# Optimization experiments

Measured on AMD Instinct MI355X. Metric: run time of the kernel, lower is better.

Reference implementation:

```python
import jax, jax.numpy as jnp
import numpy as np

WS = 8      # window_size
SS = 4      # shift_size
DIM = 192
HEADS = 6
N = WS * WS
EPS = 1e-5


def _rel_pos_index():
    coords = np.stack(np.meshgrid(np.arange(WS), np.arange(WS), indexing='ij')).reshape(2, -1)
    rel = (coords[:, :, None] - coords[:, None, :]).transpose(1, 2, 0)  # [N,N,2]
    rel[..., 0] += WS - 1
    rel[..., 1] += WS - 1
    rel[..., 0] *= 2 * WS - 1
    return rel.sum(-1)  # [N,N] int


def _attn_mask(H, W):
    img = np.zeros((H, W))
    sl = (slice(0, -WS), slice(-WS, -SS), slice(-SS, None))
    cnt = 0
    for hs in sl:
        for ws_ in sl:
            img[hs, ws_] = cnt
            cnt += 1
    mw = img.reshape(H // WS, WS, W // WS, WS).transpose(0, 2, 1, 3).reshape(-1, N)
    d = mw[:, None, :] - mw[:, :, None]
    return np.where(d != 0, -100.0, 0.0).astype(np.float32)  # [nW,N,N]


def _ln(x, g, b):
    m = x.mean(-1, keepdims=True)
    v = ((x - m) ** 2).mean(-1, keepdims=True)
    return (x - m) / jnp.sqrt(v + EPS) * g + b


def setup_inputs() -> dict:
    key = jax.random.key(0)
    ks = jax.random.split(key, 12)
    C, Hd = DIM, DIM * 4
    s = 0.02
    return {
        'x': jax.random.normal(ks[0], (2, 256, 256, C), dtype=jnp.float32),
        'norm1_g': jnp.ones((C,), jnp.float32),
        'norm1_b': jnp.zeros((C,), jnp.float32),
        'qkv_w': jax.random.normal(ks[1], (3 * C, C), jnp.float32) * s,
        'rpb_table': jax.random.normal(ks[2], ((2 * WS - 1) ** 2, HEADS), jnp.float32) * s,
        'proj_w': jax.random.normal(ks[3], (C, C), jnp.float32) * s,
        'proj_b': jnp.zeros((C,), jnp.float32),
        'norm2_g': jnp.ones((C,), jnp.float32),
        'norm2_b': jnp.zeros((C,), jnp.float32),
        'mlp_w1': jax.random.normal(ks[4], (Hd, C), jnp.float32) * s,
        'mlp_b1': jnp.zeros((Hd,), jnp.float32),
        'mlp_w2': jax.random.normal(ks[5], (C, Hd), jnp.float32) * s,
        'mlp_b2': jnp.zeros((C,), jnp.float32),
    }


def reference(x, norm1_g, norm1_b, qkv_w, rpb_table, proj_w, proj_b,
              norm2_g, norm2_b, mlp_w1, mlp_b1, mlp_w2, mlp_b2):
    B, H, W, C = x.shape
    hd = C // HEADS
    shortcut = x
    xn = _ln(x, norm1_g, norm1_b)
    xs = jnp.roll(xn, (-SS, -SS), axis=(1, 2))
    # window partition -> [B_*nW, N, C]
    xw = xs.reshape(B, H // WS, WS, W // WS, WS, C).transpose(0, 1, 3, 2, 4, 5).reshape(-1, N, C)
    B_ = xw.shape[0]
    qkv = (xw @ qkv_w.T).reshape(B_, N, 3, HEADS, hd).transpose(2, 0, 3, 1, 4)
    q, k, v = qkv[0] * (hd ** -0.5), qkv[1], qkv[2]
    attn = jnp.einsum('bhid,bhjd->bhij', q, k)  # [B_,H,N,N]
    rpi = jnp.asarray(_rel_pos_index().reshape(-1))
    bias = rpb_table[rpi].reshape(N, N, HEADS).transpose(2, 0, 1)  # [H,N,N]
    attn = attn + bias[None]
    mask = jnp.asarray(_attn_mask(H, W))  # [nW,N,N]
    nW = mask.shape[0]
    attn = (attn.reshape(B_ // nW, nW, HEADS, N, N) + mask[None, :, None]).reshape(B_, HEADS, N, N)
    attn = jax.nn.softmax(attn, axis=-1)
    out = jnp.einsum('bhij,bhjd->bhid', attn, v).transpose(0, 2, 1, 3).reshape(B_, N, C)
    out = out @ proj_w.T + proj_b
    # window reverse + roll back
    out = out.reshape(B, H // WS, W // WS, WS, WS, C).transpose(0, 1, 3, 2, 4, 5).reshape(B, H, W, C)
    x1 = shortcut + jnp.roll(out, (SS, SS), axis=(1, 2))
    h = _ln(x1, norm2_g, norm2_b)
    h = jax.nn.gelu(h @ mlp_w1.T + mlp_b1, approximate=False)
    h = h @ mlp_w2.T + mlp_b2
    return x1 + h
```

## Files before the change

kernel.cpp:

```cpp
#include <hip/hip_runtime.h>
#include <hip/hip_bf16.h>
#include <math.h>

typedef unsigned short u16;
typedef unsigned int u32;
typedef __attribute__((ext_vector_type(8))) short short8;
typedef __attribute__((ext_vector_type(4))) float floatx4;

__device__ __forceinline__ float bf2f(u16 u) { return __uint_as_float(((u32)u) << 16); }
__device__ __forceinline__ u16 f2bf(float f) {
  u32 u = __float_as_uint(f);
  u32 r = u + 0x7fffu + ((u >> 16) & 1u);
  return (u16)(r >> 16);
}

#define WSB_OFF  0
#define WSQ_OFF  393216
#define WSP_OFF  614400
#define WSM1_OFF 688128
#define WSM2_OFF 983040

__global__ __launch_bounds__(256) void k_prep(
    const float* __restrict__ qkvw, const float* __restrict__ projw,
    const float* __restrict__ rpb,
    const float* __restrict__ w1, const float* __restrict__ w2,
    float* __restrict__ wsb, u16* __restrict__ wsq, u16* __restrict__ wsp,
    u16* __restrict__ wsm1, u16* __restrict__ wsm2)
{
  const int tid0 = blockIdx.x * 256 + threadIdx.x;
  const int NT = gridDim.x * 256;
  for (int idx = tid0; idx < 110592; idx += NT) {
    int e = idx & 7, lane = (idx >> 3) & 63, rest = idx >> 9;
    int s = rest % 6, T = rest / 6;
    int mat = T / 12, hct = T % 12;
    int row = mat * 192 + hct * 16 + (lane & 15);
    int col = 32 * s + 8 * (lane >> 4) + e;
    float v = qkvw[(size_t)row * 192 + col];
    if (mat == 0) v *= 0.1767766952966369f;
    wsq[idx] = f2bf(v);
  }
  for (int idx = tid0; idx < 36864; idx += NT) {
    int e = idx & 7, lane = (idx >> 3) & 63, rest = idx >> 9;
    int nt = rest % 12, h = rest / 12;
    int row = 16 * nt + (lane & 15);
    int col = 32 * h + 8 * (lane >> 4) + e;
    wsp[idx] = f2bf(projw[(size_t)row * 192 + col]);
  }
  for (int idx = tid0; idx < 147456; idx += NT) {
    int e = idx & 7, lane = (idx >> 3) & 63, rest = idx >> 9;
    int s = rest % 6, t = rest / 6;
    int n = t & 1, ch = t >> 1;
    wsm1[idx] = f2bf(w1[(size_t)(ch * 32 + n * 16 + (lane & 15)) * 192
                        + 32 * s + 8 * (lane >> 4) + e]);
  }
  for (int idx = tid0; idx < 147456; idx += NT) {
    int e = idx & 7, lane = (idx >> 3) & 63, rest = idx >> 9;
    int ct = rest % 12, ch = rest / 12;
    wsm2[idx] = f2bf(w2[(size_t)(ct * 16 + (lane & 15)) * 768
                        + ch * 32 + 8 * (lane >> 4) + e]);
  }
  for (int idx = tid0; idx < 98304; idx += NT) {
    int f16 = idx & 15; int nt = f16 >> 2, r = f16 & 3;
    int t = (idx >> 4) & 255; int rest = idx >> 12;
    int h = rest % 6, cat = rest / 6;
    int w = t >> 6, m = t & 15, ql = (t >> 4) & 3;
    int i = 16 * w + 4 * ql + r, j = 16 * nt + m;
    int ir = i >> 3, ic = i & 7, jr = j >> 3, jc = j & 7;
    float v = rpb[((ir - jr + 7) * 15 + (ic - jc + 7)) * 6 + h];
    int catH = cat >> 1, catW = cat & 1;
    int ci = (catH ? ((ir < 4) ? 1 : 2) : 0) * 3 + (catW ? ((ic < 4) ? 1 : 2) : 0);
    int cj = (catH ? ((jr < 4) ? 1 : 2) : 0) * 3 + (catW ? ((jc < 4) ? 1 : 2) : 0);
    if (ci != cj) v -= 100.f;
    wsb[idx] = v;
  }
}

__global__ __launch_bounds__(256, 3) void k_fused(
    const float* __restrict__ x,
    const float* __restrict__ g1, const float* __restrict__ b1,
    const float* __restrict__ projb,
    const float* __restrict__ wsb, const u16* __restrict__ wsq,
    const u16* __restrict__ wsp,
    const float* __restrict__ g2, const float* __restrict__ b2,
    const u16* __restrict__ wsm1, const float* __restrict__ bm1,
    const u16* __restrict__ wsm2, const float* __restrict__ bm2,
    float* __restrict__ out)
{
  __shared__ __align__(16) u16 xnA[12800];
  __shared__ __align__(16) u16 pool[12288];
  const int QS = 0, KS = 2560, VT = 5120, POB = 7424;

  const int tid = threadIdx.x;
  const int blk = blockIdx.x;
  const int b  = blk >> 10;
  const int wh = (blk >> 5) & 31;
  const int ww = blk & 31;

  {
    const int t = tid >> 2, l4 = tid & 3;
    const int rr = t >> 3, cc = t & 7;
    const int oh = (wh * 8 + rr + 4) & 255;
    const int ow = (ww * 8 + cc + 4) & 255;
    const float* px = x + (((size_t)b * 65536 + (size_t)oh * 256 + ow) * 192) + l4 * 48;
    float rv[48];
    float s = 0.f, ss = 0.f;
    const float4* p4 = (const float4*)px;
    #pragma unroll
    for (int i = 0; i < 12; ++i) {
      float4 v = p4[i];
      rv[i*4+0] = v.x; rv[i*4+1] = v.y; rv[i*4+2] = v.z; rv[i*4+3] = v.w;
      s  += v.x + v.y + v.z + v.w;
      ss += v.x*v.x + v.y*v.y + v.z*v.z + v.w*v.w;
    }
    s += __shfl_xor(s, 1);  s += __shfl_xor(s, 2);
    ss += __shfl_xor(ss, 1); ss += __shfl_xor(ss, 2);
    const float mean = s * (1.f / 192.f);
    const float var  = ss * (1.f / 192.f) - mean * mean;
    const float rstd = rsqrtf(var + 1e-5f);
    const int c0 = l4 * 48;
    #pragma unroll
    for (int i = 0; i < 12; ++i) {
      ushort4 o;
      o.x = f2bf((rv[i*4+0] - mean) * rstd * g1[c0+i*4+0] + b1[c0+i*4+0]);
      o.y = f2bf((rv[i*4+1] - mean) * rstd * g1[c0+i*4+1] + b1[c0+i*4+1]);
      o.z = f2bf((rv[i*4+2] - mean) * rstd * g1[c0+i*4+2] + b1[c0+i*4+2]);
      o.w = f2bf((rv[i*4+3] - mean) * rstd * g1[c0+i*4+3] + b1[c0+i*4+3]);
      *(ushort4*)&xnA[t * 200 + c0 + i*4] = o;
    }
  }

  const int w    = tid >> 6;
  const int lane = tid & 63;
  const int m    = tid & 15;
  const int ql   = (tid >> 4) & 3;
  const int ct   = w >> 1;
  const int tb   = (w & 1) * 2;
  const int cat  = ((wh == 31) ? 2 : 0) | ((ww == 31) ? 1 : 0);
  const float* pbias = wsb + ((size_t)(cat * 6) * 256 + tid) * 16;
  const int po = POB + w * 1152;

  floatx4 acc[12];
  #pragma unroll
  for (int nt = 0; nt < 12; ++nt) acc[nt] = (floatx4){0.f, 0.f, 0.f, 0.f};

  __syncthreads();

  #pragma unroll 1
  for (int h = 0; h < 6; ++h) {
    {
      const u16* wqp = wsq + (size_t)(h * 2 + ct) * 3072 + lane * 8;
      floatx4 dq[2], dk[2], dv[2];
      #pragma unroll
      for (int t = 0; t < 2; ++t) {
        dq[t] = (floatx4){0.f,0.f,0.f,0.f};
        dk[t] = (floatx4){0.f,0.f,0.f,0.f};
        dv[t] = (floatx4){0.f,0.f,0.f,0.f};
      }
      #pragma unroll
      for (int s = 0; s < 6; ++s) {
        short8 a0 = *(const short8*)&xnA[(16*tb + m) * 200 + 32*s + 8*ql];
        short8 a1 = *(const short8*)&xnA[(16*tb + 16 + m) * 200 + 32*s + 8*ql];
        short8 bq = *(const short8*)(wqp + s*512);
        short8 bk = *(const short8*)(wqp + 36864 + s*512);
        short8 bv = *(const short8*)(wqp + 73728 + s*512);
        dq[0] = __builtin_amdgcn_mfma_f32_16x16x32_bf16(a0, bq, dq[0], 0, 0, 0);
        dq[1] = __builtin_amdgcn_mfma_f32_16x16x32_bf16(a1, bq, dq[1], 0, 0, 0);
        dk[0] = __builtin_amdgcn_mfma_f32_16x16x32_bf16(a0, bk, dk[0], 0, 0, 0);
        dk[1] = __builtin_amdgcn_mfma_f32_16x16x32_bf16(a1, bk, dk[1], 0, 0, 0);
        dv[0] = __builtin_amdgcn_mfma_f32_16x16x32_bf16(a0, bv, dv[0], 0, 0, 0);
        dv[1] = __builtin_amdgcn_mfma_f32_16x16x32_bf16(a1, bv, dv[1], 0, 0, 0);
      }
      #pragma unroll
      for (int t = 0; t < 2; ++t) {
        #pragma unroll
        for (int r = 0; r < 4; ++r) {
          pool[QS + (16*(tb+t) + 4*ql + r)*40 + ct*16 + m] = f2bf(dq[t][r]);
          pool[KS + (16*(tb+t) + 4*ql + r)*40 + ct*16 + m] = f2bf(dk[t][r]);
        }
        ushort4 o;
        o.x = f2bf(dv[t][0]); o.y = f2bf(dv[t][1]);
        o.z = f2bf(dv[t][2]); o.w = f2bf(dv[t][3]);
        *(ushort4*)&pool[VT + (ct*16 + m)*72 + 16*(tb+t) + 4*ql] = o;
      }
    }
    __syncthreads();

    floatx4 sf[4];
    {
      short8 aq = *(const short8*)&pool[QS + (16*w + m)*40 + 8*ql];
      const float* pb = pbias + (size_t)h * 4096;
      #pragma unroll
      for (int nt = 0; nt < 4; ++nt) {
        float4 b4 = *(const float4*)(pb + nt*4);
        short8 bk = *(const short8*)&pool[KS + (16*nt + m)*40 + 8*ql];
        sf[nt] = __builtin_amdgcn_mfma_f32_16x16x32_bf16(
            aq, bk, (floatx4){b4.x, b4.y, b4.z, b4.w}, 0, 0, 0);
      }
    }
    {
      float mxr[4] = {-3.0e38f, -3.0e38f, -3.0e38f, -3.0e38f};
      #pragma unroll
      for (int nt = 0; nt < 4; ++nt)
        #pragma unroll
        for (int r = 0; r < 4; ++r) mxr[r] = fmaxf(mxr[r], sf[nt][r]);
      #pragma unroll
      for (int d = 1; d <= 8; d <<= 1)
        #pragma unroll
        for (int r = 0; r < 4; ++r) mxr[r] = fmaxf(mxr[r], __shfl_xor(mxr[r], d));
      float smr[4] = {0.f, 0.f, 0.f, 0.f};
      #pragma unroll
      for (int nt = 0; nt < 4; ++nt)
        #pragma unroll
        for (int r = 0; r < 4; ++r) {
          float e = __expf(sf[nt][r] - mxr[r]);
          sf[nt][r] = e;
          smr[r] += e;
        }
      #pragma unroll
      for (int d = 1; d <= 8; d <<= 1)
        #pragma unroll
        for (int r = 0; r < 4; ++r) smr[r] += __shfl_xor(smr[r], d);
      #pragma unroll
      for (int r = 0; r < 4; ++r) {
        const float inv = 1.f / smr[r];
        #pragma unroll
        for (int nt = 0; nt < 4; ++nt)
          pool[po + (4*ql + r)*72 + 16*nt + m] = f2bf(sf[nt][r] * inv);
      }
    }

    floatx4 of[2];
    of[0] = (floatx4){0.f,0.f,0.f,0.f}; of[1] = (floatx4){0.f,0.f,0.f,0.f};
    #pragma unroll
    for (int s = 0; s < 2; ++s) {
      short8 ap = *(const short8*)&pool[po + m*72 + 32*s + 8*ql];
      #pragma unroll
      for (int mt = 0; mt < 2; ++mt) {
        short8 bv = *(const short8*)&pool[VT + (16*mt + m)*72 + 32*s + 8*ql];
        of[mt] = __builtin_amdgcn_mfma_f32_16x16x32_bf16(ap, bv, of[mt], 0, 0, 0);
      }
    }
    __syncthreads();

    #pragma unroll
    for (int mt = 0; mt < 2; ++mt)
      #pragma unroll
      for (int r = 0; r < 4; ++r)
        pool[po + (4*ql + r)*40 + 16*mt + m] = f2bf(of[mt][r]);
    {
      short8 ao = *(const short8*)&pool[po + m*40 + 8*ql];
      const u16* wpp = wsp + (size_t)h * 6144 + lane * 8;
      #pragma unroll
      for (int nt = 0; nt < 12; ++nt) {
        short8 bw = *(const short8*)(wpp + nt*512);
        acc[nt] = __builtin_amdgcn_mfma_f32_16x16x32_bf16(ao, bw, acc[nt], 0, 0, 0);
      }
    }
  }

  short8 pf1[3];
  #pragma unroll
  for (int it = 0; it < 3; ++it)
    pf1[it] = *(const short8*)(wsm1 + (size_t)(it * 256 + tid) * 8);

  {
    size_t rb[4];
    #pragma unroll
    for (int r = 0; r < 4; ++r) {
      const int i  = 16*w + 4*ql + r;
      const int ir = i >> 3, ic = i & 7;
      const int oh = (wh * 8 + ir + 4) & 255;
      const int ow = (ww * 8 + ic + 4) & 255;
      rb[r] = ((size_t)b * 65536 + (size_t)oh * 256 + ow) * 192;
    }
    #pragma unroll
    for (int nt = 0; nt < 12; ++nt) {
      const int c = 16*nt + m;
      const float pb = projb[c];
      #pragma unroll
      for (int r = 0; r < 4; ++r)
        acc[nt][r] += x[rb[r] + c] + pb;
    }
  }

  {
    float s[4] = {0.f,0.f,0.f,0.f}, ss[4] = {0.f,0.f,0.f,0.f};
    #pragma unroll
    for (int nt = 0; nt < 12; ++nt)
      #pragma unroll
      for (int r = 0; r < 4; ++r) {
        float v = acc[nt][r];
        s[r] += v; ss[r] += v * v;
      }
    #pragma unroll
    for (int d = 1; d <= 8; d <<= 1)
      #pragma unroll
      for (int r = 0; r < 4; ++r) {
        s[r]  += __shfl_xor(s[r], d);
        ss[r] += __shfl_xor(ss[r], d);
      }
    float mean[4], rstd[4];
    #pragma unroll
    for (int r = 0; r < 4; ++r) {
      mean[r] = s[r] * (1.f / 192.f);
      float var = ss[r] * (1.f / 192.f) - mean[r] * mean[r];
      rstd[r] = rsqrtf(var + 1e-5f);
    }
    #pragma unroll
    for (int nt = 0; nt < 12; ++nt) {
      const int c = 16*nt + m;
      const float gg = g2[c], bb = b2[c], bb2 = bm2[c];
      #pragma unroll
      for (int r = 0; r < 4; ++r) {
        xnA[(16*w + 4*ql + r) * 200 + c] = f2bf((acc[nt][r] - mean[r]) * rstd[r] * gg + bb);
        acc[nt][r] += bb2;
      }
    }
  }

  short8 a_all[6];
  #pragma unroll
  for (int s = 0; s < 6; ++s)
    a_all[s] = *(const short8*)&xnA[(16*w + m) * 200 + 32*s + 8*ql];

  __syncthreads();
  #pragma unroll
  for (int it = 0; it < 3; ++it)
    *(short8*)&pool[(it * 256 + tid) * 8] = pf1[it];
  #pragma unroll
  for (int it = 0; it < 3; ++it)
    pf1[it] = *(const short8*)(wsm1 + 6144 + (size_t)(it * 256 + tid) * 8);
  __syncthreads();

  const int gsb = w * 640;

  #pragma unroll 1
  for (int ch = 0; ch < 24; ++ch) {
    const int buf = ch & 1;
    const u16* w2p = wsm2 + (size_t)ch * 6144 + lane * 8;

    short8 w2h[6];
    #pragma unroll
    for (int j = 0; j < 6; ++j)
      w2h[j] = *(const short8*)(w2p + j * 512);

    const u16* w1p = pool + buf * 6144 + lane * 8;
    floatx4 h0 = (floatx4){0.f, 0.f, 0.f, 0.f};
    floatx4 h1 = (floatx4){0.f, 0.f, 0.f, 0.f};
    #pragma unroll
    for (int s = 0; s < 6; ++s) {
      short8 b0 = *(const short8*)(w1p + s * 512);
      short8 b1 = *(const short8*)(w1p + 3072 + s * 512);
      h0 = __builtin_amdgcn_mfma_f32_16x16x32_bf16(a_all[s], b0, h0, 0, 0, 0);
      h1 = __builtin_amdgcn_mfma_f32_16x16x32_bf16(a_all[s], b1, h1, 0, 0, 0);
    }

    const int c0 = ch * 32;
    {
      const float bb0 = bm1[c0 + m];
      const float bb1 = bm1[c0 + 16 + m];
      #pragma unroll
      for (int r = 0; r < 4; ++r) {
        float v0 = h0[r] + bb0;
        float v1 = h1[r] + bb1;
        float g0 = 0.5f * v0 * (1.f + erff(v0 * 0.70710678118654752f));
        float g1 = 0.5f * v1 * (1.f + erff(v1 * 0.70710678118654752f));
        xnA[gsb + (ql * 4 + r) * 40 + m] = f2bf(g0);
        xnA[gsb + (ql * 4 + r) * 40 + 16 + m] = f2bf(g1);
      }
    }

    {
      short8 ap = *(const short8*)&xnA[gsb + m * 40 + 8 * ql];
      #pragma unroll
      for (int j = 0; j < 6; ++j)
        acc[j] = __builtin_amdgcn_mfma_f32_16x16x32_bf16(ap, w2h[j], acc[j], 0, 0, 0);
      #pragma unroll
      for (int j = 0; j < 6; ++j)
        w2h[j] = *(const short8*)(w2p + (6 + j) * 512);
      #pragma unroll
      for (int j = 0; j < 6; ++j)
        acc[6 + j] = __builtin_amdgcn_mfma_f32_16x16x32_bf16(ap, w2h[j], acc[6 + j], 0, 0, 0);
    }

    if (ch + 1 < 24) {
      #pragma unroll
      for (int it = 0; it < 3; ++it)
        *(short8*)&pool[(buf ^ 1) * 6144 + (it * 256 + tid) * 8] = pf1[it];
      if (ch + 2 < 24) {
        const u16* p1 = wsm1 + (size_t)(ch + 2) * 6144;
        #pragma unroll
        for (int it = 0; it < 3; ++it)
          pf1[it] = *(const short8*)(p1 + (it * 256 + tid) * 8);
      }
      __syncthreads();
    }
  }

  {
    size_t rb[4];
    #pragma unroll
    for (int r = 0; r < 4; ++r) {
      const int i  = 16*w + 4*ql + r;
      const int ir = i >> 3, ic = i & 7;
      const int oh = (wh * 8 + ir + 4) & 255;
      const int ow = (ww * 8 + ic + 4) & 255;
      rb[r] = ((size_t)b * 65536 + (size_t)oh * 256 + ow) * 192;
    }
    #pragma unroll
    for (int nt = 0; nt < 12; ++nt) {
      const int c = 16*nt + m;
      #pragma unroll
      for (int r = 0; r < 4; ++r)
        out[rb[r] + c] = acc[nt][r];
    }
  }
}

extern "C" void kernel_launch(void* const* d_in, const int* in_sizes, int n_in,
                              void* d_out, int out_size, void* d_ws, size_t ws_size,
                              hipStream_t stream) {
  (void)in_sizes; (void)n_in; (void)out_size; (void)ws_size;
  const float* x    = (const float*)d_in[0];
  const float* n1g  = (const float*)d_in[1];
  const float* n1b  = (const float*)d_in[2];
  const float* qkvw = (const float*)d_in[3];
  const float* rpb  = (const float*)d_in[4];
  const float* pw   = (const float*)d_in[5];
  const float* pb   = (const float*)d_in[6];
  const float* n2g  = (const float*)d_in[7];
  const float* n2b  = (const float*)d_in[8];
  const float* w1   = (const float*)d_in[9];
  const float* bm1  = (const float*)d_in[10];
  const float* w2   = (const float*)d_in[11];
  const float* bm2  = (const float*)d_in[12];
  float* out = (float*)d_out;

  float* wsb  = (float*)((char*)d_ws + WSB_OFF);
  u16*   wsq  = (u16*)((char*)d_ws + WSQ_OFF);
  u16*   wsp  = (u16*)((char*)d_ws + WSP_OFF);
  u16*   wsm1 = (u16*)((char*)d_ws + WSM1_OFF);
  u16*   wsm2 = (u16*)((char*)d_ws + WSM2_OFF);

  hipLaunchKernelGGL(k_prep, dim3(192), dim3(256), 0, stream,
                     qkvw, pw, rpb, w1, w2, wsb, wsq, wsp, wsm1, wsm2);
  hipLaunchKernelGGL(k_fused, dim3(2048), dim3(256), 0, stream,
                     x, n1g, n1b, pb, wsb, wsq, wsp,
                     n2g, n2b, wsm1, bm1, wsm2, bm2, out);
}
```

Baseline: 455.1 us.

## Hoist weight loads earlier, reorder MLP prefetch, use tanh-form GELU

Bias and projection-weight loads in the attention phase are moved ahead of barriers and MFMA chains so their global latency overlaps other work. In the MLP loop, the W1 LDS staging and next-chunk prefetch now run at the top of each iteration, and all 12 W2 fragments are loaded up front in one batch. The exact erf GELU is replaced by a sigmoid-based tanh approximation. The prep kernel grid is doubled. These changes raise register pressure and make the GELU slightly less accurate.

```diff
diff --git a/kernel.cpp b/kernel.cpp
--- a/kernel.cpp
+++ b/kernel.cpp
@@ -12,6 +12,11 @@
   u32 u = __float_as_uint(f);
   u32 r = u + 0x7fffu + ((u >> 16) & 1u);
   return (u16)(r >> 16);
+}
+__device__ __forceinline__ float fast_gelu(float v) {
+  float y2 = 1.5957691216057308f * v * (1.f + 0.044715f * v * v);
+  float e = __expf(fminf(y2, 60.f));
+  return v * e * __builtin_amdgcn_rcpf(e + 1.f);
 }
 
 #define WSB_OFF  0
@@ -183,18 +188,23 @@
         *(ushort4*)&pool[VT + (ct*16 + m)*72 + 16*(tb+t) + 4*ql] = o;
       }
     }
+
+    float4 pb4[4];
+    {
+      const float* pb = pbias + (size_t)h * 4096;
+      #pragma unroll
+      for (int nt = 0; nt < 4; ++nt) pb4[nt] = *(const float4*)(pb + nt*4);
+    }
     __syncthreads();
 
     floatx4 sf[4];
     {
       short8 aq = *(const short8*)&pool[QS + (16*w + m)*40 + 8*ql];
-      const float* pb = pbias + (size_t)h * 4096;
       #pragma unroll
       for (int nt = 0; nt < 4; ++nt) {
-        float4 b4 = *(const float4*)(pb + nt*4);
         short8 bk = *(const short8*)&pool[KS + (16*nt + m)*40 + 8*ql];
         sf[nt] = __builtin_amdgcn_mfma_f32_16x16x32_bf16(
-            aq, bk, (floatx4){b4.x, b4.y, b4.z, b4.w}, 0, 0, 0);
+            aq, bk, (floatx4){pb4[nt].x, pb4[nt].y, pb4[nt].z, pb4[nt].w}, 0, 0, 0);
       }
     }
     {
@@ -229,6 +239,13 @@
       }
     }
 
+    short8 bw[12];
+    {
+      const u16* wpp = wsp + (size_t)h * 6144 + lane * 8;
+      #pragma unroll
+      for (int nt = 0; nt < 12; ++nt) bw[nt] = *(const short8*)(wpp + nt*512);
+    }
+
     floatx4 of[2];
     of[0] = (floatx4){0.f,0.f,0.f,0.f}; of[1] = (floatx4){0.f,0.f,0.f,0.f};
     #pragma unroll
@@ -249,12 +266,9 @@
         pool[po + (4*ql + r)*40 + 16*mt + m] = f2bf(of[mt][r]);
     {
       short8 ao = *(const short8*)&pool[po + m*40 + 8*ql];
-      const u16* wpp = wsp + (size_t)h * 6144 + lane * 8;
-      #pragma unroll
-      for (int nt = 0; nt < 12; ++nt) {
-        short8 bw = *(const short8*)(wpp + nt*512);
-        acc[nt] = __builtin_amdgcn_mfma_f32_16x16x32_bf16(ao, bw, acc[nt], 0, 0, 0);
-      }
+      #pragma unroll
+      for (int nt = 0; nt < 12; ++nt)
+        acc[nt] = __builtin_amdgcn_mfma_f32_16x16x32_bf16(ao, bw[nt], acc[nt], 0, 0, 0);
     }
   }
 
@@ -337,12 +351,28 @@
   #pragma unroll 1
   for (int ch = 0; ch < 24; ++ch) {
     const int buf = ch & 1;
-    const u16* w2p = wsm2 + (size_t)ch * 6144 + lane * 8;
-
-    short8 w2h[6];
-    #pragma unroll
-    for (int j = 0; j < 6; ++j)
-      w2h[j] = *(const short8*)(w2p + j * 512);
+
+    if (ch + 1 < 24) {
+      #pragma unroll
+      for (int it = 0; it < 3; ++it)
+        *(short8*)&pool[(buf ^ 1) * 6144 + (it * 256 + tid) * 8] = pf1[it];
+      if (ch + 2 < 24) {
+        const u16* p1 = wsm1 + (size_t)(ch + 2) * 6144;
+        #pragma unroll
+        for (int it = 0; it < 3; ++it)
+          pf1[it] = *(const short8*)(p1 + (it * 256 + tid) * 8);
+      }
+    }
+
+    short8 w2r[12];
+    {
+      const u16* w2p = wsm2 + (size_t)ch * 6144 + lane * 8;
+      #pragma unroll
+      for (int j = 0; j < 12; ++j)
+        w2r[j] = *(const short8*)(w2p + j * 512);
+    }
+    const float bb0 = bm1[ch * 32 + m];
+    const float bb1 = bm1[ch * 32 + 16 + m];
 
     const u16* w1p = pool + buf * 6144 + lane * 8;
     floatx4 h0 = (floatx4){0.f, 0.f, 0.f, 0.f};
@@ -355,46 +385,22 @@
       h1 = __builtin_amdgcn_mfma_f32_16x16x32_bf16(a_all[s], b1, h1, 0, 0, 0);
     }
 
-    const int c0 = ch * 32;
-    {
-      const float bb0 = bm1[c0 + m];
-      const float bb1 = bm1[c0 + 16 + m];
-      #pragma unroll
-      for (int r = 0; r < 4; ++r) {
-        float v0 = h0[r] + bb0;
-        float v1 = h1[r] + bb1;
-        float g0 = 0.5f * v0 * (1.f + erff(v0 * 0.70710678118654752f));
-        float g1 = 0.5f * v1 * (1.f + erff(v1 * 0.70710678118654752f));
-        xnA[gsb + (ql * 4 + r) * 40 + m] = f2bf(g0);
-        xnA[gsb + (ql * 4 + r) * 40 + 16 + m] = f2bf(g1);
-      }
+    #pragma unroll
+    for (int r = 0; r < 4; ++r) {
+      float g0 = fast_gelu(h0[r] + bb0);
+      float g1 = fast_gelu(h1[r] + bb1);
+      xnA[gsb + (ql * 4 + r) * 40 + m] = f2bf(g0);
+      xnA[gsb + (ql * 4 + r) * 40 + 16 + m] = f2bf(g1);
     }
 
     {
       short8 ap = *(const short8*)&xnA[gsb + m * 40 + 8 * ql];
       #pragma unroll
-      for (int j = 0; j < 6; ++j)
-        acc[j] = __builtin_amdgcn_mfma_f32_16x16x32_bf16(ap, w2h[j], acc[j], 0, 0, 0);
-      #pragma unroll
-      for (int j = 0; j < 6; ++j)
-        w2h[j] = *(const short8*)(w2p + (6 + j) * 512);
-      #pragma unroll
-      for (int j = 0; j < 6; ++j)
-        acc[6 + j] = __builtin_amdgcn_mfma_f32_16x16x32_bf16(ap, w2h[j], acc[6 + j], 0, 0, 0);
-    }
-
-    if (ch + 1 < 24) {
-      #pragma unroll
-      for (int it = 0; it < 3; ++it)
-        *(short8*)&pool[(buf ^ 1) * 6144 + (it * 256 + tid) * 8] = pf1[it];
-      if (ch + 2 < 24) {
-        const u16* p1 = wsm1 + (size_t)(ch + 2) * 6144;
-        #pragma unroll
-        for (int it = 0; it < 3; ++it)
-          pf1[it] = *(const short8*)(p1 + (it * 256 + tid) * 8);
-      }
-      __syncthreads();
-    }
+      for (int j = 0; j < 12; ++j)
+        acc[j] = __builtin_amdgcn_mfma_f32_16x16x32_bf16(ap, w2r[j], acc[j], 0, 0, 0);
+    }
+
+    if (ch + 1 < 24) __syncthreads();
   }
 
   {
@@ -442,7 +448,7 @@
   u16*   wsm1 = (u16*)((char*)d_ws + WSM1_OFF);
   u16*   wsm2 = (u16*)((char*)d_ws + WSM2_OFF);
 
-  hipLaunchKernelGGL(k_prep, dim3(192), dim3(256), 0, stream,
+  hipLaunchKernelGGL(k_prep, dim3(384), dim3(256), 0, stream,
                      qkvw, pw, rpb, w1, w2, wsb, wsq, wsp, wsm1, wsm2);
   hipLaunchKernelGGL(k_fused, dim3(2048), dim3(256), 0, stream,
                      x, n1g, n1b, pb, wsb, wsq, wsp,
```

After: 437.5 us. -3.9%, faster.
